# Kernel tuning notes

Measured on AMD Instinct MI355X. Metric: run time of the kernel, lower is better.

The kernel has to match this reference:

```python
import jax, jax.numpy as jnp
import numpy as np

N = 16                      # input_dim (state dimension)
EPS = 1e-6
TRIL_R, TRIL_C = np.tril_indices(N)   # 136 lower-triangular slots


def setup_inputs() -> dict:
    key = jax.random.key(0)
    ks = jax.random.split(key, 7)
    B = 131072
    def xavier(k, fan_in, fan_out):
        lim = float(np.sqrt(6.0 / (fan_in + fan_out)))
        return jax.random.uniform(k, (fan_in, fan_out), jnp.float32, -lim, lim)
    return {
        "points": jax.random.normal(ks[0], (B, N), jnp.float32),
        "W0": xavier(ks[1], N, 512),
        "b0": jax.random.normal(ks[2], (512,), jnp.float32) * 0.01,
        "W1": xavier(ks[3], 512, 512),
        "b1": jax.random.normal(ks[4], (512,), jnp.float32) * 0.01,
        "W2": xavier(ks[5], 512, 136),
        "b2": jax.random.normal(ks[6], (136,), jnp.float32) * 0.01,
    }


def reference(points, W0, b0, W1, b1, W2, b2):
    # MLP: tanh, tanh, identity
    h = jnp.tanh(points @ W0 + b0)
    h = jnp.tanh(h @ W1 + b1)
    net = h @ W2 + b2                         # [B, 136] tril entries
    B = points.shape[0]
    # Batched scatter into lower-triangular matrices M: [B, N, N]
    M = jnp.zeros((B, N, N), points.dtype).at[:, TRIL_R, TRIL_C].set(net)
    # x^T (M M^T) x == ||M^T x||^2
    y = jnp.einsum('bij,bi->bj', M, points)   # (M^T x)_j = sum_i M_ij x_i
    vals = jnp.sum(y * y, axis=-1) + EPS * jnp.sum(points * points, axis=-1)
    return vals.reshape(-1, 1)
```

## Files before the change

### kernel.cpp

```cpp
#include <hip/hip_runtime.h>

typedef __bf16 bf16x4 __attribute__((ext_vector_type(4)));
typedef __bf16 bf16x8 __attribute__((ext_vector_type(8)));
typedef float f32x16 __attribute__((ext_vector_type(16)));

#define W0F_OFF 0
#define W1F_OFF 8192
#define W2F_OFF (8192 + 262144)
#define PREP_TOTAL (8192 + 262144 + 81920)

__global__ void prep_weights(const float* __restrict__ W0,
                             const float* __restrict__ W1,
                             const float* __restrict__ W2,
                             __bf16* __restrict__ ws) {
    int t = blockIdx.x * 256 + threadIdx.x;
    if (t < 8192) {
        int j = t & 7, lane = (t >> 3) & 63, nt = t >> 9;
        int n = nt * 32 + (lane & 31);
        int k = (lane >> 5) * 8 + j;
        ws[W0F_OFF + t] = (__bf16)W0[k * 512 + n];
    } else if (t < 8192 + 262144) {
        int u = t - 8192;
        int j = u & 7, lane = (u >> 3) & 63;
        int x = u >> 9;
        int kk = x & 31, nt = x >> 5;
        int n = nt * 32 + (lane & 31);
        int k = kk * 16 + (lane >> 5) * 8 + j;
        ws[W1F_OFF + u] = (__bf16)W1[k * 512 + n];
    } else if (t < PREP_TOTAL) {
        int v = t - (8192 + 262144);
        int j = v & 7, lane = (v >> 3) & 63;
        int x = v >> 9;
        int kk = x & 31, nt = x >> 5;
        int n = nt * 32 + (lane & 31);
        int k = kk * 16 + (lane >> 5) * 8 + j;
        ws[W2F_OFF + v] = (n < 136) ? (__bf16)W2[k * 136 + n] : (__bf16)0.0f;
    }
}

__device__ __forceinline__ float fast_tanh(float x) {
#if __has_builtin(__builtin_amdgcn_exp2f)
    float e = __builtin_amdgcn_exp2f(x * 2.885390081777926f);
#else
    float e = exp2f(x * 2.885390081777926f);
#endif
    return 1.0f - 2.0f * __builtin_amdgcn_rcpf(e + 1.0f);
}

#define HSTR 520
#define NSTR 140

__global__ __launch_bounds__(512, 2)
void fused_mlp_quad(const float* __restrict__ points,
                    const float* __restrict__ b0,
                    const float* __restrict__ b1,
                    const float* __restrict__ b2,
                    const __bf16* __restrict__ ws,
                    float* __restrict__ out) {
    __shared__ __align__(16) unsigned char lds_raw[66560];
    __bf16* h  = (__bf16*)lds_raw;
    float* net = (float*)lds_raw;

    const __bf16* w0f = ws + W0F_OFF;
    const __bf16* w1f = ws + W1F_OFF;
    const __bf16* w2f = ws + W2F_OFF;

    const int tid = threadIdx.x;
    const int w   = tid >> 6;
    const int l   = tid & 63;
    const int ln  = l & 31;
    const int hi  = l >> 5;
    const int row0 = blockIdx.x * 64;

    const int lofs = l * 8;
    const int ofs16 = (blockIdx.x >> 3) & 15;
    const int ofs8  = (blockIdx.x >> 3) & 7;

    {
        bf16x8 bx[2];
#pragma unroll
        for (int bt = 0; bt < 2; ++bt) {
            const float* src = points + (row0 + bt * 32 + ln) * 16 + hi * 8;
            float4 p0 = ((const float4*)src)[0];
            float4 p1 = ((const float4*)src)[1];
            bf16x8 v;
            v[0] = (__bf16)p0.x; v[1] = (__bf16)p0.y; v[2] = (__bf16)p0.z; v[3] = (__bf16)p0.w;
            v[4] = (__bf16)p1.x; v[5] = (__bf16)p1.y; v[6] = (__bf16)p1.z; v[7] = (__bf16)p1.w;
            bx[bt] = v;
        }
#pragma unroll
        for (int t = 0; t < 2; ++t) {
            const int ntg = w * 2 + t;
            bf16x8 wf = *(const bf16x8*)(w0f + ntg * 512 + lofs);
#pragma unroll
            for (int bt = 0; bt < 2; ++bt) {
                f32x16 acc = {};
                acc = __builtin_amdgcn_mfma_f32_32x32x16_bf16(wf, bx[bt], acc, 0, 0, 0);
#pragma unroll
                for (int rg = 0; rg < 4; ++rg) {
                    const int n0 = ntg * 32 + 8 * rg + 4 * hi;
                    float4 bias = *(const float4*)(b0 + n0);
                    bf16x4 v;
                    v[0] = (__bf16)fast_tanh(acc[4 * rg + 0] + bias.x);
                    v[1] = (__bf16)fast_tanh(acc[4 * rg + 1] + bias.y);
                    v[2] = (__bf16)fast_tanh(acc[4 * rg + 2] + bias.z);
                    v[3] = (__bf16)fast_tanh(acc[4 * rg + 3] + bias.w);
                    *(bf16x4*)(h + (bt * 32 + ln) * HSTR + n0) = v;
                }
            }
        }
    }
    __syncthreads();

    f32x16 acc1[2][2] = {};
    {
        const __bf16* arow0 = h + ln * HSTR + hi * 8;
        const __bf16* arow1 = h + (32 + ln) * HSTR + hi * 8;
        const __bf16* wb0 = w1f + (w * 2 + 0) * 16384 + lofs;
        const __bf16* wb1 = w1f + (w * 2 + 1) * 16384 + lofs;
        for (int ks2 = 0; ks2 < 16; ++ks2) {
            const int ks = (ks2 + ofs16) & 15;
            bf16x8 aa[2][2], bb[2][2];
#pragma unroll
            for (int u = 0; u < 2; ++u) {
                const int kk = ks * 2 + u;
                const int vo = kk * 512;
                aa[u][0] = *(const bf16x8*)(arow0 + kk * 16);
                aa[u][1] = *(const bf16x8*)(arow1 + kk * 16);
                bb[u][0] = *(const bf16x8*)(wb0 + vo);
                bb[u][1] = *(const bf16x8*)(wb1 + vo);
            }
#pragma unroll
            for (int u = 0; u < 2; ++u) {
#pragma unroll
                for (int t = 0; t < 2; ++t) {
                    acc1[0][t] = __builtin_amdgcn_mfma_f32_32x32x16_bf16(bb[u][t], aa[u][0], acc1[0][t], 0, 0, 0);
                    acc1[1][t] = __builtin_amdgcn_mfma_f32_32x32x16_bf16(bb[u][t], aa[u][1], acc1[1][t], 0, 0, 0);
                }
            }
        }
    }
    __syncthreads();
#pragma unroll
    for (int t = 0; t < 2; ++t) {
#pragma unroll
        for (int bt = 0; bt < 2; ++bt) {
#pragma unroll
            for (int rg = 0; rg < 4; ++rg) {
                const int n0 = (w * 2 + t) * 32 + 8 * rg + 4 * hi;
                float4 bias = *(const float4*)(b1 + n0);
                bf16x4 v;
                v[0] = (__bf16)fast_tanh(acc1[bt][t][4 * rg + 0] + bias.x);
                v[1] = (__bf16)fast_tanh(acc1[bt][t][4 * rg + 1] + bias.y);
                v[2] = (__bf16)fast_tanh(acc1[bt][t][4 * rg + 2] + bias.z);
                v[3] = (__bf16)fast_tanh(acc1[bt][t][4 * rg + 3] + bias.w);
                *(bf16x4*)(h + (bt * 32 + ln) * HSTR + n0) = v;
            }
        }
    }
    __syncthreads();

    f32x16 acc2a = {}, acc2e = {};
    const int nt2 = w >> 1;
    const int bt2 = w & 1;
    const bool two = (w < 2);
    {
        const __bf16* arowA = h + (bt2 * 32 + ln) * HSTR + hi * 8;
        const __bf16* arowE = h + ((w & 1) * 32 + ln) * HSTR + hi * 8;
        const __bf16* wbA = w2f + nt2 * 16384 + lofs;
        const __bf16* wbE = w2f + 4 * 16384 + lofs;
        for (int ks2 = 0; ks2 < 8; ++ks2) {
            const int ks = (ks2 + ofs8) & 7;
            bf16x8 aaA[2], wA[2], aaE[2], wE[2];
#pragma unroll
            for (int u = 0; u < 2; ++u) {
                const int kk = ks * 4 + u * 2;
                const int vo = kk * 512;
                aaA[u] = *(const bf16x8*)(arowA + kk * 16);
                wA[u]  = *(const bf16x8*)(wbA + vo);
                if (two) {
                    aaE[u] = *(const bf16x8*)(arowE + kk * 16);
                    wE[u]  = *(const bf16x8*)(wbE + vo);
                }
            }
            bf16x8 aaA2[2], wA2[2], aaE2[2], wE2[2];
#pragma unroll
            for (int u = 0; u < 2; ++u) {
                const int kk = ks * 4 + u * 2 + 1;
                const int vo = kk * 512;
                aaA2[u] = *(const bf16x8*)(arowA + kk * 16);
                wA2[u]  = *(const bf16x8*)(wbA + vo);
                if (two) {
                    aaE2[u] = *(const bf16x8*)(arowE + kk * 16);
                    wE2[u]  = *(const bf16x8*)(wbE + vo);
                }
            }
#pragma unroll
            for (int u = 0; u < 2; ++u) {
                acc2a = __builtin_amdgcn_mfma_f32_32x32x16_bf16(wA[u], aaA[u], acc2a, 0, 0, 0);
                acc2a = __builtin_amdgcn_mfma_f32_32x32x16_bf16(wA2[u], aaA2[u], acc2a, 0, 0, 0);
                if (two) {
                    acc2e = __builtin_amdgcn_mfma_f32_32x32x16_bf16(wE[u], aaE[u], acc2e, 0, 0, 0);
                    acc2e = __builtin_amdgcn_mfma_f32_32x32x16_bf16(wE2[u], aaE2[u], acc2e, 0, 0, 0);
                }
            }
        }
    }
    __syncthreads();
    {
#pragma unroll
        for (int rg = 0; rg < 4; ++rg) {
            const int n0 = nt2 * 32 + 8 * rg + 4 * hi;
            float4 bias = *(const float4*)(b2 + n0);
            float4 v;
            v.x = acc2a[4 * rg + 0] + bias.x;
            v.y = acc2a[4 * rg + 1] + bias.y;
            v.z = acc2a[4 * rg + 2] + bias.z;
            v.w = acc2a[4 * rg + 3] + bias.w;
            *(float4*)(net + (bt2 * 32 + ln) * NSTR + n0) = v;
        }
        if (two) {
            const int n0 = 128 + 4 * hi;
            float4 bias = *(const float4*)(b2 + n0);
            float4 v;
            v.x = acc2e[0] + bias.x;
            v.y = acc2e[1] + bias.y;
            v.z = acc2e[2] + bias.z;
            v.w = acc2e[3] + bias.w;
            *(float4*)(net + ((w & 1) * 32 + ln) * NSTR + n0) = v;
        }
    }
    __syncthreads();

    {
        const int r  = tid >> 3;
        const int jg = tid & 7;
        const float* xp = points + (row0 + r) * 16;
        float xv[16];
#pragma unroll
        for (int i = 0; i < 4; ++i) {
            float4 v = ((const float4*)xp)[i];
            xv[i * 4 + 0] = v.x; xv[i * 4 + 1] = v.y;
            xv[i * 4 + 2] = v.z; xv[i * 4 + 3] = v.w;
        }
        float sumsq = 0.f;
#pragma unroll
        for (int i = 0; i < 16; ++i) sumsq += xv[i] * xv[i];
        float p = 0.f;
#pragma unroll
        for (int jj = 0; jj < 2; ++jj) {
            const int j = jg + jj * 8;
            float y = 0.f;
#pragma unroll
            for (int i = 0; i < 16; ++i) {
                float mv = net[r * NSTR + ((i * (i + 1)) >> 1) + j];
                y += (i >= j) ? mv * xv[i] : 0.f;
            }
            p += y * y;
        }
        p += __shfl_xor(p, 1);
        p += __shfl_xor(p, 2);
        p += __shfl_xor(p, 4);
        if (jg == 0) out[row0 + r] = p + 1e-6f * sumsq;
    }
}

extern "C" void kernel_launch(void* const* d_in, const int* in_sizes, int n_in,
                              void* d_out, int out_size, void* d_ws, size_t ws_size,
                              hipStream_t stream) {
    const float* points = (const float*)d_in[0];
    const float* W0 = (const float*)d_in[1];
    const float* b0 = (const float*)d_in[2];
    const float* W1 = (const float*)d_in[3];
    const float* b1 = (const float*)d_in[4];
    const float* W2 = (const float*)d_in[5];
    const float* b2 = (const float*)d_in[6];
    __bf16* ws = (__bf16*)d_ws;
    float* out = (float*)d_out;

    prep_weights<<<(PREP_TOTAL + 255) / 256, 256, 0, stream>>>(W0, W1, W2, ws);

    const int B = in_sizes[0] / 16;
    fused_mlp_quad<<<B / 64, 512, 0, stream>>>(points, b0, b1, b2, ws, out);
}
```

Measured before the change: 188.5 us.

## Double rows per block to 128 and prefetch weight fragments in layers 1-2

Each block now processes 128 rows instead of 64, so every W1/W2 weight fragment loaded from global/L2 feeds four batch tiles instead of two, halving weight traffic per row. The layer-1 and layer-2 loops software-prefetch the next k-step's weight fragments into registers while MFMAs run on the current ones, and layer 2's work split across waves is remapped. The cost is 130 KB of LDS per block, which limits each CU to one 512-thread block and reduces latency hiding. The accumulator set also doubles, raising register pressure.

```diff
diff --git a/kernel.cpp b/kernel.cpp
--- a/kernel.cpp
+++ b/kernel.cpp
@@ -57,7 +57,7 @@
                     const float* __restrict__ b2,
                     const __bf16* __restrict__ ws,
                     float* __restrict__ out) {
-    __shared__ __align__(16) unsigned char lds_raw[66560];
+    __shared__ __align__(16) unsigned char lds_raw[133120];
     __bf16* h  = (__bf16*)lds_raw;
     float* net = (float*)lds_raw;
 
@@ -70,16 +70,15 @@
     const int l   = tid & 63;
     const int ln  = l & 31;
     const int hi  = l >> 5;
-    const int row0 = blockIdx.x * 64;
+    const int row0 = blockIdx.x * 128;
 
     const int lofs = l * 8;
     const int ofs16 = (blockIdx.x >> 3) & 15;
-    const int ofs8  = (blockIdx.x >> 3) & 7;
-
-    {
-        bf16x8 bx[2];
-#pragma unroll
-        for (int bt = 0; bt < 2; ++bt) {
+
+    {
+        bf16x8 bx[4];
+#pragma unroll
+        for (int bt = 0; bt < 4; ++bt) {
             const float* src = points + (row0 + bt * 32 + ln) * 16 + hi * 8;
             float4 p0 = ((const float4*)src)[0];
             float4 p1 = ((const float4*)src)[1];
@@ -93,7 +92,7 @@
             const int ntg = w * 2 + t;
             bf16x8 wf = *(const bf16x8*)(w0f + ntg * 512 + lofs);
 #pragma unroll
-            for (int bt = 0; bt < 2; ++bt) {
+            for (int bt = 0; bt < 4; ++bt) {
                 f32x16 acc = {};
                 acc = __builtin_amdgcn_mfma_f32_32x32x16_bf16(wf, bx[bt], acc, 0, 0, 0);
 #pragma unroll
@@ -112,31 +111,47 @@
     }
     __syncthreads();
 
-    f32x16 acc1[2][2] = {};
-    {
-        const __bf16* arow0 = h + ln * HSTR + hi * 8;
-        const __bf16* arow1 = h + (32 + ln) * HSTR + hi * 8;
+    f32x16 acc1[4][2] = {};
+    {
+        const __bf16* ab = h + ln * HSTR + hi * 8;
         const __bf16* wb0 = w1f + (w * 2 + 0) * 16384 + lofs;
         const __bf16* wb1 = w1f + (w * 2 + 1) * 16384 + lofs;
+        bf16x8 nb00, nb01, nb10, nb11;
+        {
+            const int kk0 = ofs16 * 2;
+            nb00 = *(const bf16x8*)(wb0 + kk0 * 512);
+            nb01 = *(const bf16x8*)(wb1 + kk0 * 512);
+            nb10 = *(const bf16x8*)(wb0 + (kk0 + 1) * 512);
+            nb11 = *(const bf16x8*)(wb1 + (kk0 + 1) * 512);
+        }
         for (int ks2 = 0; ks2 < 16; ++ks2) {
-            const int ks = (ks2 + ofs16) & 15;
-            bf16x8 aa[2][2], bb[2][2];
+            const int ks  = (ks2 + ofs16) & 15;
+            const int ksn = (ks2 + 1 + ofs16) & 15;
+            const bf16x8 bb00 = nb00, bb01 = nb01, bb10 = nb10, bb11 = nb11;
+            bf16x8 aa[2][4];
 #pragma unroll
             for (int u = 0; u < 2; ++u) {
-                const int kk = ks * 2 + u;
-                const int vo = kk * 512;
-                aa[u][0] = *(const bf16x8*)(arow0 + kk * 16);
-                aa[u][1] = *(const bf16x8*)(arow1 + kk * 16);
-                bb[u][0] = *(const bf16x8*)(wb0 + vo);
-                bb[u][1] = *(const bf16x8*)(wb1 + vo);
-            }
-#pragma unroll
-            for (int u = 0; u < 2; ++u) {
-#pragma unroll
-                for (int t = 0; t < 2; ++t) {
-                    acc1[0][t] = __builtin_amdgcn_mfma_f32_32x32x16_bf16(bb[u][t], aa[u][0], acc1[0][t], 0, 0, 0);
-                    acc1[1][t] = __builtin_amdgcn_mfma_f32_32x32x16_bf16(bb[u][t], aa[u][1], acc1[1][t], 0, 0, 0);
-                }
+                const int ko = (ks * 2 + u) * 16;
+#pragma unroll
+                for (int bt = 0; bt < 4; ++bt)
+                    aa[u][bt] = *(const bf16x8*)(ab + bt * 32 * HSTR + ko);
+            }
+            {
+                const int kk0 = ksn * 2;
+                nb00 = *(const bf16x8*)(wb0 + kk0 * 512);
+                nb01 = *(const bf16x8*)(wb1 + kk0 * 512);
+                nb10 = *(const bf16x8*)(wb0 + (kk0 + 1) * 512);
+                nb11 = *(const bf16x8*)(wb1 + (kk0 + 1) * 512);
+            }
+#pragma unroll
+            for (int bt = 0; bt < 4; ++bt) {
+                acc1[bt][0] = __builtin_amdgcn_mfma_f32_32x32x16_bf16(bb00, aa[0][bt], acc1[bt][0], 0, 0, 0);
+                acc1[bt][1] = __builtin_amdgcn_mfma_f32_32x32x16_bf16(bb01, aa[0][bt], acc1[bt][1], 0, 0, 0);
+            }
+#pragma unroll
+            for (int bt = 0; bt < 4; ++bt) {
+                acc1[bt][0] = __builtin_amdgcn_mfma_f32_32x32x16_bf16(bb10, aa[1][bt], acc1[bt][0], 0, 0, 0);
+                acc1[bt][1] = __builtin_amdgcn_mfma_f32_32x32x16_bf16(bb11, aa[1][bt], acc1[bt][1], 0, 0, 0);
             }
         }
     }
@@ -144,7 +159,7 @@
 #pragma unroll
     for (int t = 0; t < 2; ++t) {
 #pragma unroll
-        for (int bt = 0; bt < 2; ++bt) {
+        for (int bt = 0; bt < 4; ++bt) {
 #pragma unroll
             for (int rg = 0; rg < 4; ++rg) {
                 const int n0 = (w * 2 + t) * 32 + 8 * rg + 4 * hi;
@@ -160,108 +175,134 @@
     }
     __syncthreads();
 
-    f32x16 acc2a = {}, acc2e = {};
-    const int nt2 = w >> 1;
-    const int bt2 = w & 1;
-    const bool two = (w < 2);
-    {
-        const __bf16* arowA = h + (bt2 * 32 + ln) * HSTR + hi * 8;
-        const __bf16* arowE = h + ((w & 1) * 32 + ln) * HSTR + hi * 8;
-        const __bf16* wbA = w2f + nt2 * 16384 + lofs;
-        const __bf16* wbE = w2f + 4 * 16384 + lofs;
-        for (int ks2 = 0; ks2 < 8; ++ks2) {
-            const int ks = (ks2 + ofs8) & 7;
-            bf16x8 aaA[2], wA[2], aaE[2], wE[2];
-#pragma unroll
-            for (int u = 0; u < 2; ++u) {
-                const int kk = ks * 4 + u * 2;
-                const int vo = kk * 512;
-                aaA[u] = *(const bf16x8*)(arowA + kk * 16);
-                wA[u]  = *(const bf16x8*)(wbA + vo);
-                if (two) {
-                    aaE[u] = *(const bf16x8*)(arowE + kk * 16);
-                    wE[u]  = *(const bf16x8*)(wbE + vo);
+    f32x16 acc2[3] = {};
+    const bool three = (w < 4);
+    const int my_bt = three ? w : (w - 4);
+    const int ntb   = three ? 0 : 3;
+    {
+        const __bf16* arow2 = h + (my_bt * 32 + ln) * HSTR + hi * 8;
+        const __bf16* wq0 = w2f + (ntb + 0) * 16384 + lofs;
+        const __bf16* wq1 = w2f + (ntb + 1) * 16384 + lofs;
+        const __bf16* wq2 = w2f + 2 * 16384 + lofs;
+        bf16x8 nw00, nw01, nw10, nw11;
+        bf16x8 nw02 = {}, nw12 = {};
+        {
+            const int kk0 = ofs16 * 2;
+            nw00 = *(const bf16x8*)(wq0 + kk0 * 512);
+            nw01 = *(const bf16x8*)(wq1 + kk0 * 512);
+            nw10 = *(const bf16x8*)(wq0 + (kk0 + 1) * 512);
+            nw11 = *(const bf16x8*)(wq1 + (kk0 + 1) * 512);
+            if (three) {
+                nw02 = *(const bf16x8*)(wq2 + kk0 * 512);
+                nw12 = *(const bf16x8*)(wq2 + (kk0 + 1) * 512);
+            }
+        }
+        for (int ks2 = 0; ks2 < 16; ++ks2) {
+            const int ks  = (ks2 + ofs16) & 15;
+            const int ksn = (ks2 + 1 + ofs16) & 15;
+            const bf16x8 b00 = nw00, b01 = nw01, b02 = nw02;
+            const bf16x8 b10 = nw10, b11 = nw11, b12 = nw12;
+            bf16x8 aa0 = *(const bf16x8*)(arow2 + (ks * 2 + 0) * 16);
+            bf16x8 aa1 = *(const bf16x8*)(arow2 + (ks * 2 + 1) * 16);
+            {
+                const int kk0 = ksn * 2;
+                nw00 = *(const bf16x8*)(wq0 + kk0 * 512);
+                nw01 = *(const bf16x8*)(wq1 + kk0 * 512);
+                nw10 = *(const bf16x8*)(wq0 + (kk0 + 1) * 512);
+                nw11 = *(const bf16x8*)(wq1 + (kk0 + 1) * 512);
+                if (three) {
+                    nw02 = *(const bf16x8*)(wq2 + kk0 * 512);
+                    nw12 = *(const bf16x8*)(wq2 + (kk0 + 1) * 512);
                 }
             }
-            bf16x8 aaA2[2], wA2[2], aaE2[2], wE2[2];
-#pragma unroll
-            for (int u = 0; u < 2; ++u) {
-                const int kk = ks * 4 + u * 2 + 1;
-                const int vo = kk * 512;
-                aaA2[u] = *(const bf16x8*)(arowA + kk * 16);
-                wA2[u]  = *(const bf16x8*)(wbA + vo);
-                if (two) {
-                    aaE2[u] = *(const bf16x8*)(arowE + kk * 16);
-                    wE2[u]  = *(const bf16x8*)(wbE + vo);
+            acc2[0] = __builtin_amdgcn_mfma_f32_32x32x16_bf16(b00, aa0, acc2[0], 0, 0, 0);
+            acc2[1] = __builtin_amdgcn_mfma_f32_32x32x16_bf16(b01, aa0, acc2[1], 0, 0, 0);
+            if (three)
+                acc2[2] = __builtin_amdgcn_mfma_f32_32x32x16_bf16(b02, aa0, acc2[2], 0, 0, 0);
+            acc2[0] = __builtin_amdgcn_mfma_f32_32x32x16_bf16(b10, aa1, acc2[0], 0, 0, 0);
+            acc2[1] = __builtin_amdgcn_mfma_f32_32x32x16_bf16(b11, aa1, acc2[1], 0, 0, 0);
+            if (three)
+                acc2[2] = __builtin_amdgcn_mfma_f32_32x32x16_bf16(b12, aa1, acc2[2], 0, 0, 0);
+        }
+    }
+    __syncthreads();
+    {
+        const int r = my_bt * 32 + ln;
+        if (three) {
+#pragma unroll
+            for (int q = 0; q < 3; ++q) {
+#pragma unroll
+                for (int rg = 0; rg < 4; ++rg) {
+                    const int n0 = q * 32 + 8 * rg + 4 * hi;
+                    float4 bias = *(const float4*)(b2 + n0);
+                    float4 v;
+                    v.x = acc2[q][4 * rg + 0] + bias.x;
+                    v.y = acc2[q][4 * rg + 1] + bias.y;
+                    v.z = acc2[q][4 * rg + 2] + bias.z;
+                    v.w = acc2[q][4 * rg + 3] + bias.w;
+                    *(float4*)(net + r * NSTR + n0) = v;
                 }
             }
-#pragma unroll
-            for (int u = 0; u < 2; ++u) {
-                acc2a = __builtin_amdgcn_mfma_f32_32x32x16_bf16(wA[u], aaA[u], acc2a, 0, 0, 0);
-                acc2a = __builtin_amdgcn_mfma_f32_32x32x16_bf16(wA2[u], aaA2[u], acc2a, 0, 0, 0);
-                if (two) {
-                    acc2e = __builtin_amdgcn_mfma_f32_32x32x16_bf16(wE[u], aaE[u], acc2e, 0, 0, 0);
-                    acc2e = __builtin_amdgcn_mfma_f32_32x32x16_bf16(wE2[u], aaE2[u], acc2e, 0, 0, 0);
+        } else {
+#pragma unroll
+            for (int rg = 0; rg < 4; ++rg) {
+                const int n0 = 96 + 8 * rg + 4 * hi;
+                float4 bias = *(const float4*)(b2 + n0);
+                float4 v;
+                v.x = acc2[0][4 * rg + 0] + bias.x;
+                v.y = acc2[0][4 * rg + 1] + bias.y;
+                v.z = acc2[0][4 * rg + 2] + bias.z;
+                v.w = acc2[0][4 * rg + 3] + bias.w;
+                *(float4*)(net + r * NSTR + n0) = v;
+            }
+            {
+                const int n0 = 128 + 4 * hi;
+                float4 bias = *(const float4*)(b2 + n0);
+                float4 v;
+                v.x = acc2[1][0] + bias.x;
+                v.y = acc2[1][1] + bias.y;
+                v.z = acc2[1][2] + bias.z;
+                v.w = acc2[1][3] + bias.w;
+                *(float4*)(net + r * NSTR + n0) = v;
+            }
+        }
+    }
+    __syncthreads();
+
+    {
+        const int r8 = tid >> 3;
+        const int jg = tid & 7;
+#pragma unroll
+        for (int half = 0; half < 2; ++half) {
+            const int r = r8 + half * 64;
+            const float* xp = points + (row0 + r) * 16;
+            float xv[16];
+#pragma unroll
+            for (int i = 0; i < 4; ++i) {
+                float4 v = ((const float4*)xp)[i];
+                xv[i * 4 + 0] = v.x; xv[i * 4 + 1] = v.y;
+                xv[i * 4 + 2] = v.z; xv[i * 4 + 3] = v.w;
+            }
+            float sumsq = 0.f;
+#pragma unroll
+            for (int i = 0; i < 16; ++i) sumsq += xv[i] * xv[i];
+            float p = 0.f;
+#pragma unroll
+            for (int jj = 0; jj < 2; ++jj) {
+                const int j = jg + jj * 8;
+                float y = 0.f;
+#pragma unroll
+                for (int i = 0; i < 16; ++i) {
+                    float mv = net[r * NSTR + ((i * (i + 1)) >> 1) + j];
+                    y += (i >= j) ? mv * xv[i] : 0.f;
                 }
-            }
-        }
-    }
-    __syncthreads();
-    {
-#pragma unroll
-        for (int rg = 0; rg < 4; ++rg) {
-            const int n0 = nt2 * 32 + 8 * rg + 4 * hi;
-            float4 bias = *(const float4*)(b2 + n0);
-            float4 v;
-            v.x = acc2a[4 * rg + 0] + bias.x;
-            v.y = acc2a[4 * rg + 1] + bias.y;
-            v.z = acc2a[4 * rg + 2] + bias.z;
-            v.w = acc2a[4 * rg + 3] + bias.w;
-            *(float4*)(net + (bt2 * 32 + ln) * NSTR + n0) = v;
-        }
-        if (two) {
-            const int n0 = 128 + 4 * hi;
-            float4 bias = *(const float4*)(b2 + n0);
-            float4 v;
-            v.x = acc2e[0] + bias.x;
-            v.y = acc2e[1] + bias.y;
-            v.z = acc2e[2] + bias.z;
-            v.w = acc2e[3] + bias.w;
-            *(float4*)(net + ((w & 1) * 32 + ln) * NSTR + n0) = v;
-        }
-    }
-    __syncthreads();
-
-    {
-        const int r  = tid >> 3;
-        const int jg = tid & 7;
-        const float* xp = points + (row0 + r) * 16;
-        float xv[16];
-#pragma unroll
-        for (int i = 0; i < 4; ++i) {
-            float4 v = ((const float4*)xp)[i];
-            xv[i * 4 + 0] = v.x; xv[i * 4 + 1] = v.y;
-            xv[i * 4 + 2] = v.z; xv[i * 4 + 3] = v.w;
-        }
-        float sumsq = 0.f;
-#pragma unroll
-        for (int i = 0; i < 16; ++i) sumsq += xv[i] * xv[i];
-        float p = 0.f;
-#pragma unroll
-        for (int jj = 0; jj < 2; ++jj) {
-            const int j = jg + jj * 8;
-            float y = 0.f;
-#pragma unroll
-            for (int i = 0; i < 16; ++i) {
-                float mv = net[r * NSTR + ((i * (i + 1)) >> 1) + j];
-                y += (i >= j) ? mv * xv[i] : 0.f;
-            }
-            p += y * y;
-        }
-        p += __shfl_xor(p, 1);
-        p += __shfl_xor(p, 2);
-        p += __shfl_xor(p, 4);
-        if (jg == 0) out[row0 + r] = p + 1e-6f * sumsq;
+                p += y * y;
+            }
+            p += __shfl_xor(p, 1);
+            p += __shfl_xor(p, 2);
+            p += __shfl_xor(p, 4);
+            if (jg == 0) out[row0 + r] = p + 1e-6f * sumsq;
+        }
     }
 }
 
@@ -281,5 +322,5 @@
     prep_weights<<<(PREP_TOTAL + 255) / 256, 256, 0, stream>>>(W0, W1, W2, ws);
 
     const int B = in_sizes[0] / 16;
-    fused_mlp_quad<<<B / 64, 512, 0, stream>>>(points, b0, b1, b2, ws, out);
+    fused_mlp_quad<<<B / 128, 512, 0, stream>>>(points, b0, b1, b2, ws, out);
 }
```

New measurement: 191.1 us. Within noise of the previous version (+1.4%).

## Process two 64-row sub-batches per block with staggered wave-group software pipelining

Applied to the files above, without the earlier changes.

Each block now handles 128 rows as two 64-row halves held in a doubled LDS buffer. Waves 0-3 and 4-7 run the phases in opposite order: one group does the MFMA matmul for one half while the other does the tanh/bias epilogue for the other half, so matrix and vector work overlap. Layer 2 is restructured so five waves each own one 32-column tile, replacing the former split with an extra tile on two waves. The weight-prep kernel is rewritten to write one bf16x8 vector per lane. The 130KB LDS allocation cuts occupancy to one block per CU, which may undercut the intended overlap.

```diff
diff --git a/kernel.cpp b/kernel.cpp
--- a/kernel.cpp
+++ b/kernel.cpp
@@ -7,35 +7,25 @@
 #define W0F_OFF 0
 #define W1F_OFF 8192
 #define W2F_OFF (8192 + 262144)
-#define PREP_TOTAL (8192 + 262144 + 81920)
 
 __global__ void prep_weights(const float* __restrict__ W0,
                              const float* __restrict__ W1,
                              const float* __restrict__ W2,
                              __bf16* __restrict__ ws) {
-    int t = blockIdx.x * 256 + threadIdx.x;
-    if (t < 8192) {
-        int j = t & 7, lane = (t >> 3) & 63, nt = t >> 9;
-        int n = nt * 32 + (lane & 31);
-        int k = (lane >> 5) * 8 + j;
-        ws[W0F_OFF + t] = (__bf16)W0[k * 512 + n];
-    } else if (t < 8192 + 262144) {
-        int u = t - 8192;
-        int j = u & 7, lane = (u >> 3) & 63;
-        int x = u >> 9;
-        int kk = x & 31, nt = x >> 5;
-        int n = nt * 32 + (lane & 31);
-        int k = kk * 16 + (lane >> 5) * 8 + j;
-        ws[W1F_OFF + u] = (__bf16)W1[k * 512 + n];
-    } else if (t < PREP_TOTAL) {
-        int v = t - (8192 + 262144);
-        int j = v & 7, lane = (v >> 3) & 63;
-        int x = v >> 9;
-        int kk = x & 31, nt = x >> 5;
-        int n = nt * 32 + (lane & 31);
-        int k = kk * 16 + (lane >> 5) * 8 + j;
-        ws[W2F_OFF + v] = (n < 136) ? (__bf16)W2[k * 136 + n] : (__bf16)0.0f;
-    }
+    const int wave = blockIdx.x * 8 + (threadIdx.x >> 6);
+    const int l   = threadIdx.x & 63;
+    const int col = l & 31, kh = l >> 5;
+    const float* src; int nt, kk, S, nlim;
+    if (wave < 16)       { src = W0; nt = wave; kk = 0;          S = 512; nlim = 512; }
+    else if (wave < 528) { int r = wave - 16;  src = W1; nt = r >> 5; kk = r & 31; S = 512; nlim = 512; }
+    else                 { int r = wave - 528; src = W2; nt = r >> 5; kk = r & 31; S = 136; nlim = 136; }
+    const int n  = nt * 32 + col;
+    const int k0 = kk * 16 + kh * 8;
+    bf16x8 v;
+#pragma unroll
+    for (int j = 0; j < 8; ++j)
+        v[j] = (n < nlim) ? (__bf16)src[(k0 + j) * S + n] : (__bf16)0.0f;
+    *(bf16x8*)(ws + wave * 512 + l * 8) = v;
 }
 
 __device__ __forceinline__ float fast_tanh(float x) {
@@ -57,7 +47,7 @@
                     const float* __restrict__ b2,
                     const __bf16* __restrict__ ws,
                     float* __restrict__ out) {
-    __shared__ __align__(16) unsigned char lds_raw[66560];
+    __shared__ __align__(16) unsigned char lds_raw[133120];
     __bf16* h  = (__bf16*)lds_raw;
     float* net = (float*)lds_raw;
 
@@ -70,17 +60,19 @@
     const int l   = tid & 63;
     const int ln  = l & 31;
     const int hi  = l >> 5;
-    const int row0 = blockIdx.x * 64;
+    const int row0 = blockIdx.x * 128;
 
     const int lofs = l * 8;
     const int ofs16 = (blockIdx.x >> 3) & 15;
-    const int ofs8  = (blockIdx.x >> 3) & 7;
-
-    {
+
+    const f32x16 fzero = {};
+
+
+    auto PH0 = [&](int gb) {
         bf16x8 bx[2];
 #pragma unroll
         for (int bt = 0; bt < 2; ++bt) {
-            const float* src = points + (row0 + bt * 32 + ln) * 16 + hi * 8;
+            const float* src = points + (row0 + gb + bt * 32 + ln) * 16 + hi * 8;
             float4 p0 = ((const float4*)src)[0];
             float4 p1 = ((const float4*)src)[1];
             bf16x8 v;
@@ -105,17 +97,19 @@
                     v[1] = (__bf16)fast_tanh(acc[4 * rg + 1] + bias.y);
                     v[2] = (__bf16)fast_tanh(acc[4 * rg + 2] + bias.z);
                     v[3] = (__bf16)fast_tanh(acc[4 * rg + 3] + bias.w);
-                    *(bf16x4*)(h + (bt * 32 + ln) * HSTR + n0) = v;
-                }
-            }
-        }
-    }
-    __syncthreads();
-
-    f32x16 acc1[2][2] = {};
-    {
-        const __bf16* arow0 = h + ln * HSTR + hi * 8;
-        const __bf16* arow1 = h + (32 + ln) * HSTR + hi * 8;
+                    *(bf16x4*)(h + (gb + bt * 32 + ln) * HSTR + n0) = v;
+                }
+            }
+        }
+    };
+
+    auto P1M = [&](int gb, f32x16 (&acc1)[2][2]) {
+#pragma unroll
+        for (int bt = 0; bt < 2; ++bt)
+#pragma unroll
+            for (int t = 0; t < 2; ++t) acc1[bt][t] = fzero;
+        const __bf16* arow0 = h + (gb + ln) * HSTR + hi * 8;
+        const __bf16* arow1 = h + (gb + 32 + ln) * HSTR + hi * 8;
         const __bf16* wb0 = w1f + (w * 2 + 0) * 16384 + lofs;
         const __bf16* wb1 = w1f + (w * 2 + 1) * 16384 + lofs;
         for (int ks2 = 0; ks2 < 16; ++ks2) {
@@ -124,11 +118,10 @@
 #pragma unroll
             for (int u = 0; u < 2; ++u) {
                 const int kk = ks * 2 + u;
-                const int vo = kk * 512;
                 aa[u][0] = *(const bf16x8*)(arow0 + kk * 16);
                 aa[u][1] = *(const bf16x8*)(arow1 + kk * 16);
-                bb[u][0] = *(const bf16x8*)(wb0 + vo);
-                bb[u][1] = *(const bf16x8*)(wb1 + vo);
+                bb[u][0] = *(const bf16x8*)(wb0 + kk * 512);
+                bb[u][1] = *(const bf16x8*)(wb1 + kk * 512);
             }
 #pragma unroll
             for (int u = 0; u < 2; ++u) {
@@ -139,101 +132,73 @@
                 }
             }
         }
-    }
-    __syncthreads();
-#pragma unroll
-    for (int t = 0; t < 2; ++t) {
-#pragma unroll
-        for (int bt = 0; bt < 2; ++bt) {
-#pragma unroll
-            for (int rg = 0; rg < 4; ++rg) {
-                const int n0 = (w * 2 + t) * 32 + 8 * rg + 4 * hi;
-                float4 bias = *(const float4*)(b1 + n0);
-                bf16x4 v;
-                v[0] = (__bf16)fast_tanh(acc1[bt][t][4 * rg + 0] + bias.x);
-                v[1] = (__bf16)fast_tanh(acc1[bt][t][4 * rg + 1] + bias.y);
-                v[2] = (__bf16)fast_tanh(acc1[bt][t][4 * rg + 2] + bias.z);
-                v[3] = (__bf16)fast_tanh(acc1[bt][t][4 * rg + 3] + bias.w);
-                *(bf16x4*)(h + (bt * 32 + ln) * HSTR + n0) = v;
-            }
-        }
-    }
-    __syncthreads();
-
-    f32x16 acc2a = {}, acc2e = {};
-    const int nt2 = w >> 1;
-    const int bt2 = w & 1;
-    const bool two = (w < 2);
-    {
-        const __bf16* arowA = h + (bt2 * 32 + ln) * HSTR + hi * 8;
-        const __bf16* arowE = h + ((w & 1) * 32 + ln) * HSTR + hi * 8;
-        const __bf16* wbA = w2f + nt2 * 16384 + lofs;
-        const __bf16* wbE = w2f + 4 * 16384 + lofs;
-        for (int ks2 = 0; ks2 < 8; ++ks2) {
-            const int ks = (ks2 + ofs8) & 7;
-            bf16x8 aaA[2], wA[2], aaE[2], wE[2];
-#pragma unroll
-            for (int u = 0; u < 2; ++u) {
-                const int kk = ks * 4 + u * 2;
-                const int vo = kk * 512;
-                aaA[u] = *(const bf16x8*)(arowA + kk * 16);
-                wA[u]  = *(const bf16x8*)(wbA + vo);
-                if (two) {
-                    aaE[u] = *(const bf16x8*)(arowE + kk * 16);
-                    wE[u]  = *(const bf16x8*)(wbE + vo);
-                }
-            }
-            bf16x8 aaA2[2], wA2[2], aaE2[2], wE2[2];
-#pragma unroll
-            for (int u = 0; u < 2; ++u) {
-                const int kk = ks * 4 + u * 2 + 1;
-                const int vo = kk * 512;
-                aaA2[u] = *(const bf16x8*)(arowA + kk * 16);
-                wA2[u]  = *(const bf16x8*)(wbA + vo);
-                if (two) {
-                    aaE2[u] = *(const bf16x8*)(arowE + kk * 16);
-                    wE2[u]  = *(const bf16x8*)(wbE + vo);
-                }
-            }
-#pragma unroll
-            for (int u = 0; u < 2; ++u) {
-                acc2a = __builtin_amdgcn_mfma_f32_32x32x16_bf16(wA[u], aaA[u], acc2a, 0, 0, 0);
-                acc2a = __builtin_amdgcn_mfma_f32_32x32x16_bf16(wA2[u], aaA2[u], acc2a, 0, 0, 0);
-                if (two) {
-                    acc2e = __builtin_amdgcn_mfma_f32_32x32x16_bf16(wE[u], aaE[u], acc2e, 0, 0, 0);
-                    acc2e = __builtin_amdgcn_mfma_f32_32x32x16_bf16(wE2[u], aaE2[u], acc2e, 0, 0, 0);
-                }
-            }
-        }
-    }
-    __syncthreads();
-    {
-#pragma unroll
-        for (int rg = 0; rg < 4; ++rg) {
-            const int n0 = nt2 * 32 + 8 * rg + 4 * hi;
-            float4 bias = *(const float4*)(b2 + n0);
-            float4 v;
-            v.x = acc2a[4 * rg + 0] + bias.x;
-            v.y = acc2a[4 * rg + 1] + bias.y;
-            v.z = acc2a[4 * rg + 2] + bias.z;
-            v.w = acc2a[4 * rg + 3] + bias.w;
-            *(float4*)(net + (bt2 * 32 + ln) * NSTR + n0) = v;
-        }
-        if (two) {
-            const int n0 = 128 + 4 * hi;
-            float4 bias = *(const float4*)(b2 + n0);
-            float4 v;
-            v.x = acc2e[0] + bias.x;
-            v.y = acc2e[1] + bias.y;
-            v.z = acc2e[2] + bias.z;
-            v.w = acc2e[3] + bias.w;
-            *(float4*)(net + ((w & 1) * 32 + ln) * NSTR + n0) = v;
-        }
-    }
-    __syncthreads();
-
-    {
-        const int r  = tid >> 3;
+    };
+
+    auto P1E = [&](int gb, f32x16 (&acc1)[2][2]) {
+#pragma unroll
+        for (int t = 0; t < 2; ++t)
+#pragma unroll
+            for (int bt = 0; bt < 2; ++bt)
+#pragma unroll
+                for (int rg = 0; rg < 4; ++rg) {
+                    const int n0 = (w * 2 + t) * 32 + 8 * rg + 4 * hi;
+                    float4 bias = *(const float4*)(b1 + n0);
+                    bf16x4 v;
+                    v[0] = (__bf16)fast_tanh(acc1[bt][t][4 * rg + 0] + bias.x);
+                    v[1] = (__bf16)fast_tanh(acc1[bt][t][4 * rg + 1] + bias.y);
+                    v[2] = (__bf16)fast_tanh(acc1[bt][t][4 * rg + 2] + bias.z);
+                    v[3] = (__bf16)fast_tanh(acc1[bt][t][4 * rg + 3] + bias.w);
+                    *(bf16x4*)(h + (gb + bt * 32 + ln) * HSTR + n0) = v;
+                }
+    };
+
+    auto P2M = [&](int gb, f32x16 (&acc2)[2]) {
+        acc2[0] = fzero; acc2[1] = fzero;
+        if (w < 5) {
+            const __bf16* arow0 = h + (gb + ln) * HSTR + hi * 8;
+            const __bf16* arow1 = h + (gb + 32 + ln) * HSTR + hi * 8;
+            const __bf16* wq = w2f + w * 16384 + lofs;
+            for (int ks2 = 0; ks2 < 16; ++ks2) {
+                const int ks = (ks2 + ofs16) & 15;
+                bf16x8 wv[2], a0[2], a1[2];
+#pragma unroll
+                for (int u = 0; u < 2; ++u) {
+                    const int kk = ks * 2 + u;
+                    wv[u] = *(const bf16x8*)(wq + kk * 512);
+                    a0[u] = *(const bf16x8*)(arow0 + kk * 16);
+                    a1[u] = *(const bf16x8*)(arow1 + kk * 16);
+                }
+#pragma unroll
+                for (int u = 0; u < 2; ++u) {
+                    acc2[0] = __builtin_amdgcn_mfma_f32_32x32x16_bf16(wv[u], a0[u], acc2[0], 0, 0, 0);
+                    acc2[1] = __builtin_amdgcn_mfma_f32_32x32x16_bf16(wv[u], a1[u], acc2[1], 0, 0, 0);
+                }
+            }
+        }
+    };
+
+    auto P2E = [&](int gb, f32x16 (&acc2)[2]) {
+        if (w < 5) {
+#pragma unroll
+            for (int bt = 0; bt < 2; ++bt)
+#pragma unroll
+                for (int rg = 0; rg < 4; ++rg) {
+                    const int n0 = w * 32 + 8 * rg + 4 * hi;
+                    if (n0 < 136) {
+                        float4 bias = *(const float4*)(b2 + n0);
+                        float4 v;
+                        v.x = acc2[bt][4 * rg + 0] + bias.x;
+                        v.y = acc2[bt][4 * rg + 1] + bias.y;
+                        v.z = acc2[bt][4 * rg + 2] + bias.z;
+                        v.w = acc2[bt][4 * rg + 3] + bias.w;
+                        *(float4*)(net + (gb + bt * 32 + ln) * NSTR + n0) = v;
+                    }
+                }
+        }
+    };
+
+    auto PH3 = [&](int gb) {
+        const int r  = gb + (tid >> 3);
         const int jg = tid & 7;
         const float* xp = points + (row0 + r) * 16;
         float xv[16];
@@ -262,7 +227,30 @@
         p += __shfl_xor(p, 2);
         p += __shfl_xor(p, 4);
         if (jg == 0) out[row0 + r] = p + 1e-6f * sumsq;
-    }
+    };
+
+#define SEP asm volatile("" ::: "memory")
+
+    f32x16 acc_a[2][2], acc_b[2][2], acc2_a[2], acc2_b[2];
+
+    PH0(0);
+    __syncthreads();
+    if (w < 4) { P1M(0, acc_a); SEP; PH0(64); }
+    else       { PH0(64); SEP; P1M(0, acc_a); }
+    __syncthreads();
+    if (w < 4) { P1M(64, acc_b); SEP; P1E(0, acc_a); }
+    else       { P1E(0, acc_a); SEP; P1M(64, acc_b); }
+    __syncthreads();
+    if (w < 4) { P2M(0, acc2_a); SEP; P1E(64, acc_b); }
+    else       { P1E(64, acc_b); SEP; P2M(0, acc2_a); }
+    __syncthreads();
+    if (w < 4) { P2M(64, acc2_b); SEP; P2E(0, acc2_a); }
+    else       { P2E(0, acc2_a); SEP; P2M(64, acc2_b); }
+    __syncthreads();
+    P2E(64, acc2_b); SEP; PH3(0);
+    __syncthreads();
+    PH3(64);
+#undef SEP
 }
 
 extern "C" void kernel_launch(void* const* d_in, const int* in_sizes, int n_in,
@@ -278,8 +266,8 @@
     __bf16* ws = (__bf16*)d_ws;
     float* out = (float*)d_out;
 
-    prep_weights<<<(PREP_TOTAL + 255) / 256, 256, 0, stream>>>(W0, W1, W2, ws);
+    prep_weights<<<86, 512, 0, stream>>>(W0, W1, W2, ws);
 
     const int B = in_sizes[0] / 16;
-    fused_mlp_quad<<<B / 64, 512, 0, stream>>>(points, b0, b1, b2, ws, out);
-}
+    fused_mlp_quad<<<B / 128, 512, 0, stream>>>(points, b0, b1, b2, ws, out);
+}
```

Result: slower. 203.2 us (+7.8%).
